# Optimization experiments

Measured on AMD Instinct MI355X. Metric: run time of the kernel, lower is better.

The kernel has to match this reference:

```python
import jax, jax.numpy as jnp
import numpy as np

D_MAX = 0.5      # max_dist init kwarg
EPS_W = 1e-8     # weight for far edges
EPS_L = 1e-5     # diagonal jitter on projected Laplacian


def setup_inputs() -> dict:
    key = jax.random.key(0)
    k1, k2, k3, k4, k5 = jax.random.split(key, 5)
    V, d_feat, E, K = 8192, 128, 262144, 512
    # scale so squared distances straddle D_MAX (both branches taken)
    inputs = jax.random.normal(k1, (V, d_feat), dtype=jnp.float32) * 0.05
    src = jax.random.randint(k2, (E,), 0, V)
    off = jax.random.randint(k3, (E,), 1, V)  # avoid self-loops
    dst = (src + off) % V
    edge_index = jnp.stack([src, dst]).astype(jnp.int32)
    A = jax.random.normal(k4, (K, K), dtype=jnp.float32)
    targets = A @ A.T / K + jnp.eye(K, dtype=jnp.float32)  # SPD covariance
    pmat = jax.random.normal(k5, (K, V), dtype=jnp.float32) / np.float32(np.sqrt(V))
    return {"inputs": inputs, "targets": targets, "edge_index": edge_index, "pmat": pmat}


def reference(inputs, targets, edge_index, pmat):
    V = inputs.shape[0]
    K = pmat.shape[0]
    src, dst = edge_index[0], edge_index[1]
    # vectorized per-edge squared distance + thresholded weight
    d = jnp.sum((inputs[src] - inputs[dst]) ** 2, axis=-1)            # [E]
    w = jnp.where(d <= D_MAX, jnp.exp(-d), jnp.float32(EPS_W))        # [E]
    # W = I on diag, w on (i,j) and (j,i) for edges, 0 elsewhere
    W = jnp.eye(V, dtype=inputs.dtype).at[src, dst].set(w).at[dst, src].set(w)
    deg = W.sum(axis=1)                                               # [V]
    idx = jnp.arange(V)
    L = (-W).at[idx, idx].add(deg)                                    # Laplacian D - W
    L_adj = (pmat @ L) @ pmat.T + EPS_L * jnp.eye(K, dtype=inputs.dtype)
    # log det(inv(L_adj)) = -logdet(L_adj); trace(L_adj @ S0) = sum(L_adj * S0^T)
    logdet_Ladj = jnp.linalg.slogdet(L_adj)[1]
    logdet_S0 = jnp.linalg.slogdet(targets)[1]
    tr = jnp.sum(L_adj * targets.T)
    return -logdet_Ladj - logdet_S0 - jnp.float32(K) + tr
```

## Files before the change

kernel.cpp:

```cpp
#include <hip/hip_runtime.h>
#include <math.h>

#define V_N 8192
#define D_F 128
#define E_N 262144
#define K_N 512
#define DMAXF 0.5f
#define EPSW 1e-8f
#define EPSL 1e-5f
#define MAX_SE 16384
#define NZ_SYRK 24
#define L68 68

#define NB_TR 1024
#define NB_CP 256
#define NB_ED (E_N / 32)

__global__ __launch_bounds__(256) void k_pre(const float* __restrict__ P, float* __restrict__ PT,
                                             const float* __restrict__ X, const int* __restrict__ ei,
                                             int* __restrict__ cnt, int* __restrict__ si,
                                             int* __restrict__ sj, float* __restrict__ sw,
                                             unsigned* __restrict__ htab,
                                             const float* __restrict__ T, float* __restrict__ Lw1) {
  int b = blockIdx.x, tid = threadIdx.x;
  if (b < NB_TR) {
    __shared__ float tl[64][65];
    int v0 = (b & 127) * 64, k0 = (b >> 7) * 64;
    int c4 = tid & 15, rq = tid >> 4;
#pragma unroll
    for (int rr = 0; rr < 4; ++rr) {
      int r = rq + 16 * rr;
      float4 f = *(const float4*)&P[(size_t)(k0 + r) * V_N + v0 + c4 * 4];
      tl[r][c4 * 4 + 0] = f.x; tl[r][c4 * 4 + 1] = f.y;
      tl[r][c4 * 4 + 2] = f.z; tl[r][c4 * 4 + 3] = f.w;
    }
    __syncthreads();
#pragma unroll
    for (int rr = 0; rr < 4; ++rr) {
      int r = rq + 16 * rr;
      float4 f;
      f.x = tl[c4 * 4 + 0][r]; f.y = tl[c4 * 4 + 1][r];
      f.z = tl[c4 * 4 + 2][r]; f.w = tl[c4 * 4 + 3][r];
      *(float4*)&PT[(size_t)(v0 + r) * K_N + k0 + c4 * 4] = f;
    }
  } else if (b < NB_TR + NB_CP) {
    int idx = (b - NB_TR) * 256 + tid;
    ((float4*)Lw1)[idx] = ((const float4*)T)[idx];
  } else {
    int t = (b - NB_TR - NB_CP) * 256 + tid;
    int e = t >> 3, lane = t & 7;
    int i = ei[e], j = ei[E_N + e];
    const float4* xi = (const float4*)(X + (size_t)i * D_F);
    const float4* xj = (const float4*)(X + (size_t)j * D_F);
    float4 A0 = xi[lane * 4 + 0], A1 = xi[lane * 4 + 1], A2 = xi[lane * 4 + 2], A3 = xi[lane * 4 + 3];
    float4 B0 = xj[lane * 4 + 0], B1 = xj[lane * 4 + 1], B2 = xj[lane * 4 + 2], B3 = xj[lane * 4 + 3];
    float d = 0.f, dx;
    dx = A0.x - B0.x; d += dx * dx; dx = A0.y - B0.y; d += dx * dx;
    dx = A0.z - B0.z; d += dx * dx; dx = A0.w - B0.w; d += dx * dx;
    dx = A1.x - B1.x; d += dx * dx; dx = A1.y - B1.y; d += dx * dx;
    dx = A1.z - B1.z; d += dx * dx; dx = A1.w - B1.w; d += dx * dx;
    dx = A2.x - B2.x; d += dx * dx; dx = A2.y - B2.y; d += dx * dx;
    dx = A2.z - B2.z; d += dx * dx; dx = A2.w - B2.w; d += dx * dx;
    dx = A3.x - B3.x; d += dx * dx; dx = A3.y - B3.y; d += dx * dx;
    dx = A3.z - B3.z; d += dx * dx; dx = A3.w - B3.w; d += dx * dx;
    d += __shfl_xor(d, 1);
    d += __shfl_xor(d, 2);
    d += __shfl_xor(d, 4);
    if (lane == 0 && d <= DMAXF) {
      float w = expf(-d);
      unsigned a = (unsigned)min(i, j), bb = (unsigned)max(i, j);
      unsigned key = a * 8192u + bb;
      unsigned h = (key * 2654435761u) >> 16;
      bool isnew = false;
      for (int probe = 0; probe < 65536; ++probe) {
        unsigned slot = (h + (unsigned)probe) & 65535u;
        unsigned prev = atomicCAS(&htab[slot], 0u, key);
        if (prev == 0u) { isnew = true; break; }
        if (prev == key) break;
      }
      if (isnew) {
        int p = atomicAdd(cnt, 1);
        if (p < MAX_SE) { si[p] = i; sj[p] = j; sw[p] = w; }
      }
    }
  }
}

__global__ __launch_bounds__(256) void k_syrk(const int* __restrict__ cnt, const int* __restrict__ si,
                                              const int* __restrict__ sj, const float* __restrict__ sw,
                                              const float* __restrict__ PT, float* __restrict__ La,
                                              const float* __restrict__ T, float* __restrict__ tr) {
  int p = blockIdx.x, bj = 0;
  while (p >= 8 - bj) { p -= 8 - bj; ++bj; }
  int bi = bj + p;
  int r0g = bi * 64, c0g = bj * 64;
  int m = min(*cnt, MAX_SE);
  int chunk = (m + NZ_SYRK - 1) / NZ_SYRK;
  int e0 = blockIdx.y * chunk;
  int e1 = min(m, e0 + chunk);

  __shared__ float As[16][68];
  __shared__ float Bs[16][68];
  int tid = threadIdx.x;
  int le = tid >> 4, f = tid & 15;
  int r0 = (tid >> 4) * 4, c0 = (tid & 15) * 4;
  float acc[4][4];
#pragma unroll
  for (int i = 0; i < 4; ++i)
#pragma unroll
    for (int j = 0; j < 4; ++j) acc[i][j] = 0.f;

  float w_ = 0.f;
  float4 ai = make_float4(0.f, 0.f, 0.f, 0.f), aj = ai, ci = ai, cj = ai;
  {
    int e = e0 + le;
    if (e < e1) {
      int i = si[e], j = sj[e];
      w_ = sw[e];
      const float* pi = &PT[(size_t)i * K_N];
      const float* pj = &PT[(size_t)j * K_N];
      ai = *(const float4*)(pi + r0g + f * 4);
      aj = *(const float4*)(pj + r0g + f * 4);
      if (bi != bj) {
        ci = *(const float4*)(pi + c0g + f * 4);
        cj = *(const float4*)(pj + c0g + f * 4);
      }
    }
  }

  for (int es = e0; es < e1; es += 16) {
    float sq = sqrtf(w_);
    float4 qa, qb;
    qa.x = sq * (ai.x - aj.x); qa.y = sq * (ai.y - aj.y);
    qa.z = sq * (ai.z - aj.z); qa.w = sq * (ai.w - aj.w);
    if (bi != bj) {
      qb.x = sq * (ci.x - cj.x); qb.y = sq * (ci.y - cj.y);
      qb.z = sq * (ci.z - cj.z); qb.w = sq * (ci.w - cj.w);
    } else {
      qb = qa;
    }
    __syncthreads();
    *(float4*)&As[le][f * 4] = qa;
    *(float4*)&Bs[le][f * 4] = qb;
    __syncthreads();

    {
      int e = es + 16 + le;
      w_ = 0.f;
      if (e < e1) {
        int i = si[e], j = sj[e];
        w_ = sw[e];
        const float* pi = &PT[(size_t)i * K_N];
        const float* pj = &PT[(size_t)j * K_N];
        ai = *(const float4*)(pi + r0g + f * 4);
        aj = *(const float4*)(pj + r0g + f * 4);
        if (bi != bj) {
          ci = *(const float4*)(pi + c0g + f * 4);
          cj = *(const float4*)(pj + c0g + f * 4);
        }
      }
    }

#pragma unroll
    for (int k = 0; k < 16; ++k) {
      float4 av = *(const float4*)&As[k][r0];
      float4 bv = *(const float4*)&Bs[k][c0];
      acc[0][0] += av.x * bv.x; acc[0][1] += av.x * bv.y; acc[0][2] += av.x * bv.z; acc[0][3] += av.x * bv.w;
      acc[1][0] += av.y * bv.x; acc[1][1] += av.y * bv.y; acc[1][2] += av.y * bv.z; acc[1][3] += av.y * bv.w;
      acc[2][0] += av.z * bv.x; acc[2][1] += av.z * bv.y; acc[2][2] += av.z * bv.z; acc[2][3] += av.z * bv.w;
      acc[3][0] += av.w * bv.x; acc[3][1] += av.w * bv.y; acc[3][2] += av.w * bv.z; acc[3][3] += av.w * bv.w;
    }
  }

  bool addeps = (blockIdx.y == 0) && (bi == bj);
  float tdot = 0.f;
#pragma unroll
  for (int i = 0; i < 4; ++i)
#pragma unroll
    for (int j = 0; j < 4; ++j) {
      float v = acc[i][j];
      int rg = r0g + r0 + i, cg = c0g + c0 + j;
      if (addeps && rg == cg) v += EPSL;
      atomicAdd(&La[(size_t)rg * K_N + cg], v);
      float sc = (bi != bj) ? 2.f : (rg == cg ? 1.f : (rg > cg ? 2.f : 0.f));
      if (sc != 0.f) tdot += sc * v * T[(size_t)rg * K_N + cg];
    }
  tdot += __shfl_down(tdot, 32); tdot += __shfl_down(tdot, 16); tdot += __shfl_down(tdot, 8);
  tdot += __shfl_down(tdot, 4);  tdot += __shfl_down(tdot, 2);  tdot += __shfl_down(tdot, 1);
  if ((tid & 63) == 0) atomicAdd(tr, tdot);
}

__device__ __forceinline__ void factor64_lds(const float* __restrict__ smF, float* A, int j0,
                                             float* __restrict__ ldout, int lane) {
  float a[64];
#pragma unroll
  for (int qq = 0; qq < 16; ++qq) {
    float4 f = *(const float4*)&smF[lane * L68 + qq * 4];
    a[qq * 4 + 0] = f.x; a[qq * 4 + 1] = f.y; a[qq * 4 + 2] = f.z; a[qq * 4 + 3] = f.w;
  }
  float ls = 0.f;
#pragma unroll
  for (int c = 0; c < 64; ++c) {
    float dc = __shfl(a[c], c);
    ls += logf(dc);
    float rs = rsqrtf(dc);
    a[c] *= rs;
#pragma unroll
    for (int k = c + 1; k < 64; ++k)
      a[k] -= a[c] * __shfl(a[c], k);
  }
#pragma unroll
  for (int qq = 0; qq < 16; ++qq) {
    float4 f;
    f.x = a[qq * 4 + 0]; f.y = a[qq * 4 + 1]; f.z = a[qq * 4 + 2]; f.w = a[qq * 4 + 3];
    *(float4*)&A[(size_t)(j0 + lane) * K_N + j0 + qq * 4] = f;
  }
  if (lane == 0) *ldout = ls;
}

__global__ __launch_bounds__(64) void k_fact0(float* La, float* Lw1, float* __restrict__ ld) {
  int m = blockIdx.x;
  float* A = m ? Lw1 : La;
  int lane = threadIdx.x;
  float a[64];
#pragma unroll
  for (int qq = 0; qq < 16; ++qq) {
    float4 f = *(const float4*)&A[(size_t)lane * K_N + qq * 4];
    a[qq * 4 + 0] = f.x; a[qq * 4 + 1] = f.y; a[qq * 4 + 2] = f.z; a[qq * 4 + 3] = f.w;
  }
  float ls = 0.f;
#pragma unroll
  for (int c = 0; c < 64; ++c) {
    float dc = __shfl(a[c], c);
    ls += logf(dc);
    float rs = rsqrtf(dc);
    a[c] *= rs;
#pragma unroll
    for (int k = c + 1; k < 64; ++k)
      a[k] -= a[c] * __shfl(a[c], k);
  }
#pragma unroll
  for (int qq = 0; qq < 16; ++qq) {
    float4 f;
    f.x = a[qq * 4 + 0]; f.y = a[qq * 4 + 1]; f.z = a[qq * 4 + 2]; f.w = a[qq * 4 + 3];
    *(float4*)&A[(size_t)lane * K_N + qq * 4] = f;
  }
  if (lane == 0) ld[m * 8] = ls;
}

__global__ __launch_bounds__(256, 1) void k_cstep(float* La, float* Lw1, float* __restrict__ ld, int s) {
  int m = blockIdx.y;
  float* A = m ? Lw1 : La;
  int tid = threadIdx.x;
  int nt2 = 7 - s;
  int q = blockIdx.x, lbj = 0;
  while (q >= nt2 - lbj) { q -= nt2 - lbj; ++lbj; }
  int lbi = lbj + q;
  int i = s + 1 + lbi, j = s + 1 + lbj;

  __shared__ float LT[64 * L68];
  __shared__ float PiT[64 * L68];
  __shared__ float PjT[64 * L68];
  __shared__ float rinv[64];

  for (int idx = tid; idx < 1024; idx += 256) {
    int r = idx >> 4, cq = (idx & 15) << 2;
    float4 f = *(const float4*)&A[(size_t)(s * 64 + r) * K_N + s * 64 + cq];
    LT[(cq + 0) * L68 + r] = f.x; LT[(cq + 1) * L68 + r] = f.y;
    LT[(cq + 2) * L68 + r] = f.z; LT[(cq + 3) * L68 + r] = f.w;
  }
  __syncthreads();
  if (tid < 64) rinv[tid] = 1.0f / LT[tid * L68 + tid];
  __syncthreads();

  {
    int w = tid >> 6, r = tid & 63;
    bool act = (w == 0) || (w == 1 && i != j);
    if (act) {
      int rowblk = (w == 0) ? i : j;
      const float* src = &A[(size_t)(rowblk * 64 + r) * K_N + s * 64];
      float x[64];
#pragma unroll
      for (int qq = 0; qq < 16; ++qq) {
        float4 f = *(const float4*)(src + qq * 4);
        x[qq * 4 + 0] = f.x; x[qq * 4 + 1] = f.y; x[qq * 4 + 2] = f.z; x[qq * 4 + 3] = f.w;
      }
#pragma unroll
      for (int c = 0; c < 64; ++c) {
        float xc = x[c] * rinv[c];
        x[c] = xc;
#pragma unroll
        for (int k = c + 1; k < 64; ++k)
          x[k] -= xc * LT[c * L68 + k];
      }
      float* dst = (w == 0) ? PiT : PjT;
#pragma unroll
      for (int k = 0; k < 64; ++k) dst[k * L68 + r] = x[k];
    }
  }
  __syncthreads();

  const float* Bp = (i == j) ? PiT : PjT;
  int r0 = (tid >> 4) * 4, c0 = (tid & 15) * 4;
  float acc[4][4];
#pragma unroll
  for (int ii = 0; ii < 4; ++ii)
#pragma unroll
    for (int jj = 0; jj < 4; ++jj) acc[ii][jj] = 0.f;
#pragma unroll 8
  for (int k = 0; k < 64; ++k) {
    float4 av = *(const float4*)&PiT[k * L68 + r0];
    float4 bv = *(const float4*)&Bp[k * L68 + c0];
    acc[0][0] += av.x * bv.x; acc[0][1] += av.x * bv.y; acc[0][2] += av.x * bv.z; acc[0][3] += av.x * bv.w;
    acc[1][0] += av.y * bv.x; acc[1][1] += av.y * bv.y; acc[1][2] += av.y * bv.z; acc[1][3] += av.y * bv.w;
    acc[2][0] += av.z * bv.x; acc[2][1] += av.z * bv.y; acc[2][2] += av.z * bv.z; acc[2][3] += av.z * bv.w;
    acc[3][0] += av.w * bv.x; acc[3][1] += av.w * bv.y; acc[3][2] += av.w * bv.z; acc[3][3] += av.w * bv.w;
  }

  if (i != j || i > s + 1) {
#pragma unroll
    for (int ii = 0; ii < 4; ++ii) {
      float* cp = &A[(size_t)(i * 64 + r0 + ii) * K_N + j * 64 + c0];
      float4 o = *(const float4*)cp;
      float4 wv;
      wv.x = o.x - acc[ii][0]; wv.y = o.y - acc[ii][1];
      wv.z = o.z - acc[ii][2]; wv.w = o.w - acc[ii][3];
      *(float4*)cp = wv;
    }
  } else {
#pragma unroll
    for (int ii = 0; ii < 4; ++ii) {
      const float* cp = &A[(size_t)(i * 64 + r0 + ii) * K_N + i * 64 + c0];
      float4 o = *(const float4*)cp;
      LT[(r0 + ii) * L68 + c0 + 0] = o.x - acc[ii][0];
      LT[(r0 + ii) * L68 + c0 + 1] = o.y - acc[ii][1];
      LT[(r0 + ii) * L68 + c0 + 2] = o.z - acc[ii][2];
      LT[(r0 + ii) * L68 + c0 + 3] = o.w - acc[ii][3];
    }
    __syncthreads();
    if (tid < 64)
      factor64_lds(LT, A, i * 64, &ld[m * 8 + s + 1], tid);
  }
}

__global__ void k_combine(const float* __restrict__ ld, const float* __restrict__ tr, float* __restrict__ out) {
  float l0 = 0.f, l1 = 0.f;
#pragma unroll
  for (int s = 0; s < 8; ++s) { l0 += ld[s]; l1 += ld[8 + s]; }
  out[0] = -l0 - l1 - (float)K_N + tr[0];
}

extern "C" void kernel_launch(void* const* d_in, const int* in_sizes, int n_in,
                              void* d_out, int out_size, void* d_ws, size_t ws_size,
                              hipStream_t stream) {
  const float* X  = (const float*)d_in[0];
  const float* T  = (const float*)d_in[1];
  const int*   ei = (const int*)d_in[2];
  const float* P  = (const float*)d_in[3];
  float* out = (float*)d_out;
  char* ws = (char*)d_ws;

  int*      cnt    = (int*)(ws + 0);
  float*    tr     = (float*)(ws + 16);
  float*    ld     = (float*)(ws + 32);
  unsigned* htab   = (unsigned*)(ws + 4096);
  float*    La     = (float*)(ws + 266240);
  float*    Lw1    = (float*)(ws + 1314816);
  int*      si     = (int*)(ws + 2363392);
  int*      sj     = (int*)(ws + 2428928);
  float*    sw     = (float*)(ws + 2494464);
  float*    PT     = (float*)(ws + 2560000);

  hipMemsetAsync(ws, 0, 1314816, stream);

  k_pre<<<NB_TR + NB_CP + NB_ED, 256, 0, stream>>>(P, PT, X, ei, cnt, si, sj, sw, htab, T, Lw1);
  k_syrk<<<dim3(36, NZ_SYRK), 256, 0, stream>>>(cnt, si, sj, sw, PT, La, T, tr);

  k_fact0<<<2, 64, 0, stream>>>(La, Lw1, ld);
  for (int s = 0; s < 7; ++s) {
    int nt2 = 7 - s;
    k_cstep<<<dim3(nt2 * (nt2 + 1) / 2, 2), 256, 0, stream>>>(La, Lw1, ld, s);
  }
  k_combine<<<1, 1, 0, stream>>>(ld, tr, out);
}
```

Before: 549.8 us.

## Enlarge SYRK tiles to 128x128 and split Cholesky step into TRSM and update kernels

The SYRK kernel now computes 128x128 output tiles with an 8x8 per-thread micro-tile, which cuts redundant gathers of projected rows. It doubles the edge-split factor to keep the grid occupied and hoists the sqrt of the weights out of the loop. The blocked Cholesky step is split into a per-block-row TRSM kernel followed by an update kernel, so each panel is solved once instead of being recomputed in every update tile. This adds an extra launch per step and raises register pressure in SYRK.

```diff
diff --git a/kernel.cpp b/kernel.cpp
--- a/kernel.cpp
+++ b/kernel.cpp
@@ -9,7 +9,7 @@
 #define EPSW 1e-8f
 #define EPSL 1e-5f
 #define MAX_SE 16384
-#define NZ_SYRK 24
+#define NZ_SYRK 48
 #define L68 68
 
 #define NB_TR 1024
@@ -91,57 +91,69 @@
                                               const float* __restrict__ PT, float* __restrict__ La,
                                               const float* __restrict__ T, float* __restrict__ tr) {
   int p = blockIdx.x, bj = 0;
-  while (p >= 8 - bj) { p -= 8 - bj; ++bj; }
+  while (p >= 4 - bj) { p -= 4 - bj; ++bj; }
   int bi = bj + p;
-  int r0g = bi * 64, c0g = bj * 64;
+  int r0g = bi * 128, c0g = bj * 128;
+  bool diag = (bi == bj);
   int m = min(*cnt, MAX_SE);
   int chunk = (m + NZ_SYRK - 1) / NZ_SYRK;
   int e0 = blockIdx.y * chunk;
   int e1 = min(m, e0 + chunk);
 
-  __shared__ float As[16][68];
-  __shared__ float Bs[16][68];
+  __shared__ float As[16][132];
+  __shared__ float Bs[16][132];
   int tid = threadIdx.x;
-  int le = tid >> 4, f = tid & 15;
-  int r0 = (tid >> 4) * 4, c0 = (tid & 15) * 4;
-  float acc[4][4];
-#pragma unroll
-  for (int i = 0; i < 4; ++i)
-#pragma unroll
-    for (int j = 0; j < 4; ++j) acc[i][j] = 0.f;
+  int le = tid >> 4, f2 = tid & 15;
+  int r0 = (tid >> 4) * 8, c0 = (tid & 15) * 8;
+  float acc[8][8];
+#pragma unroll
+  for (int ii = 0; ii < 8; ++ii)
+#pragma unroll
+    for (int jj = 0; jj < 8; ++jj) acc[ii][jj] = 0.f;
 
   float w_ = 0.f;
-  float4 ai = make_float4(0.f, 0.f, 0.f, 0.f), aj = ai, ci = ai, cj = ai;
+  float4 z4 = make_float4(0.f, 0.f, 0.f, 0.f);
+  float4 ra0 = z4, ra1 = z4, rb0 = z4, rb1 = z4;
+  float4 ca0 = z4, ca1 = z4, cb0 = z4, cb1 = z4;
   {
     int e = e0 + le;
     if (e < e1) {
       int i = si[e], j = sj[e];
-      w_ = sw[e];
+      w_ = sqrtf(sw[e]);
       const float* pi = &PT[(size_t)i * K_N];
       const float* pj = &PT[(size_t)j * K_N];
-      ai = *(const float4*)(pi + r0g + f * 4);
-      aj = *(const float4*)(pj + r0g + f * 4);
-      if (bi != bj) {
-        ci = *(const float4*)(pi + c0g + f * 4);
-        cj = *(const float4*)(pj + c0g + f * 4);
+      ra0 = *(const float4*)(pi + r0g + f2 * 8);
+      ra1 = *(const float4*)(pi + r0g + f2 * 8 + 4);
+      rb0 = *(const float4*)(pj + r0g + f2 * 8);
+      rb1 = *(const float4*)(pj + r0g + f2 * 8 + 4);
+      if (!diag) {
+        ca0 = *(const float4*)(pi + c0g + f2 * 8);
+        ca1 = *(const float4*)(pi + c0g + f2 * 8 + 4);
+        cb0 = *(const float4*)(pj + c0g + f2 * 8);
+        cb1 = *(const float4*)(pj + c0g + f2 * 8 + 4);
       }
     }
   }
 
   for (int es = e0; es < e1; es += 16) {
-    float sq = sqrtf(w_);
-    float4 qa, qb;
-    qa.x = sq * (ai.x - aj.x); qa.y = sq * (ai.y - aj.y);
-    qa.z = sq * (ai.z - aj.z); qa.w = sq * (ai.w - aj.w);
-    if (bi != bj) {
-      qb.x = sq * (ci.x - cj.x); qb.y = sq * (ci.y - cj.y);
-      qb.z = sq * (ci.z - cj.z); qb.w = sq * (ci.w - cj.w);
-    } else {
-      qb = qa;
+    float4 qa0, qa1, qb0, qb1;
+    qa0.x = w_ * (ra0.x - rb0.x); qa0.y = w_ * (ra0.y - rb0.y);
+    qa0.z = w_ * (ra0.z - rb0.z); qa0.w = w_ * (ra0.w - rb0.w);
+    qa1.x = w_ * (ra1.x - rb1.x); qa1.y = w_ * (ra1.y - rb1.y);
+    qa1.z = w_ * (ra1.z - rb1.z); qa1.w = w_ * (ra1.w - rb1.w);
+    if (!diag) {
+      qb0.x = w_ * (ca0.x - cb0.x); qb0.y = w_ * (ca0.y - cb0.y);
+      qb0.z = w_ * (ca0.z - cb0.z); qb0.w = w_ * (ca0.w - cb0.w);
+      qb1.x = w_ * (ca1.x - cb1.x); qb1.y = w_ * (ca1.y - cb1.y);
+      qb1.z = w_ * (ca1.z - cb1.z); qb1.w = w_ * (ca1.w - cb1.w);
     }
     __syncthreads();
-    *(float4*)&As[le][f * 4] = qa;
-    *(float4*)&Bs[le][f * 4] = qb;
+    *(float4*)&As[le][f2 * 8] = qa0;
+    *(float4*)&As[le][f2 * 8 + 4] = qa1;
+    if (!diag) {
+      *(float4*)&Bs[le][f2 * 8] = qb0;
+      *(float4*)&Bs[le][f2 * 8 + 4] = qb1;
+    }
     __syncthreads();
 
     {
@@ -149,40 +161,53 @@
       w_ = 0.f;
       if (e < e1) {
         int i = si[e], j = sj[e];
-        w_ = sw[e];
+        w_ = sqrtf(sw[e]);
         const float* pi = &PT[(size_t)i * K_N];
         const float* pj = &PT[(size_t)j * K_N];
-        ai = *(const float4*)(pi + r0g + f * 4);
-        aj = *(const float4*)(pj + r0g + f * 4);
-        if (bi != bj) {
-          ci = *(const float4*)(pi + c0g + f * 4);
-          cj = *(const float4*)(pj + c0g + f * 4);
+        ra0 = *(const float4*)(pi + r0g + f2 * 8);
+        ra1 = *(const float4*)(pi + r0g + f2 * 8 + 4);
+        rb0 = *(const float4*)(pj + r0g + f2 * 8);
+        rb1 = *(const float4*)(pj + r0g + f2 * 8 + 4);
+        if (!diag) {
+          ca0 = *(const float4*)(pi + c0g + f2 * 8);
+          ca1 = *(const float4*)(pi + c0g + f2 * 8 + 4);
+          cb0 = *(const float4*)(pj + c0g + f2 * 8);
+          cb1 = *(const float4*)(pj + c0g + f2 * 8 + 4);
         }
       }
     }
 
+    const float(*Bp)[132] = diag ? As : Bs;
 #pragma unroll
     for (int k = 0; k < 16; ++k) {
-      float4 av = *(const float4*)&As[k][r0];
-      float4 bv = *(const float4*)&Bs[k][c0];
-      acc[0][0] += av.x * bv.x; acc[0][1] += av.x * bv.y; acc[0][2] += av.x * bv.z; acc[0][3] += av.x * bv.w;
-      acc[1][0] += av.y * bv.x; acc[1][1] += av.y * bv.y; acc[1][2] += av.y * bv.z; acc[1][3] += av.y * bv.w;
-      acc[2][0] += av.z * bv.x; acc[2][1] += av.z * bv.y; acc[2][2] += av.z * bv.z; acc[2][3] += av.z * bv.w;
-      acc[3][0] += av.w * bv.x; acc[3][1] += av.w * bv.y; acc[3][2] += av.w * bv.z; acc[3][3] += av.w * bv.w;
-    }
-  }
-
-  bool addeps = (blockIdx.y == 0) && (bi == bj);
+      float av[8], bv[8];
+      float4 a0 = *(const float4*)&As[k][r0];
+      float4 a1 = *(const float4*)&As[k][r0 + 4];
+      float4 b0 = *(const float4*)&Bp[k][c0];
+      float4 b1 = *(const float4*)&Bp[k][c0 + 4];
+      av[0] = a0.x; av[1] = a0.y; av[2] = a0.z; av[3] = a0.w;
+      av[4] = a1.x; av[5] = a1.y; av[6] = a1.z; av[7] = a1.w;
+      bv[0] = b0.x; bv[1] = b0.y; bv[2] = b0.z; bv[3] = b0.w;
+      bv[4] = b1.x; bv[5] = b1.y; bv[6] = b1.z; bv[7] = b1.w;
+#pragma unroll
+      for (int ii = 0; ii < 8; ++ii)
+#pragma unroll
+        for (int jj = 0; jj < 8; ++jj)
+          acc[ii][jj] += av[ii] * bv[jj];
+    }
+  }
+
+  bool addeps = (blockIdx.y == 0) && diag;
   float tdot = 0.f;
 #pragma unroll
-  for (int i = 0; i < 4; ++i)
-#pragma unroll
-    for (int j = 0; j < 4; ++j) {
-      float v = acc[i][j];
-      int rg = r0g + r0 + i, cg = c0g + c0 + j;
+  for (int ii = 0; ii < 8; ++ii)
+#pragma unroll
+    for (int jj = 0; jj < 8; ++jj) {
+      float v = acc[ii][jj];
+      int rg = r0g + r0 + ii, cg = c0g + c0 + jj;
       if (addeps && rg == cg) v += EPSL;
       atomicAdd(&La[(size_t)rg * K_N + cg], v);
-      float sc = (bi != bj) ? 2.f : (rg == cg ? 1.f : (rg > cg ? 2.f : 0.f));
+      float sc = !diag ? 2.f : (rg == cg ? 1.f : (rg > cg ? 2.f : 0.f));
       if (sc != 0.f) tdot += sc * v * T[(size_t)rg * K_N + cg];
     }
   tdot += __shfl_down(tdot, 32); tdot += __shfl_down(tdot, 16); tdot += __shfl_down(tdot, 8);
@@ -248,7 +273,55 @@
   if (lane == 0) ld[m * 8] = ls;
 }
 
-__global__ __launch_bounds__(256, 1) void k_cstep(float* La, float* Lw1, float* __restrict__ ld, int s) {
+__global__ __launch_bounds__(64) void k_trsm(float* La, float* Lw1, int s) {
+  int m = blockIdx.y;
+  float* A = m ? Lw1 : La;
+  int i = s + 1 + blockIdx.x;
+  int lane = threadIdx.x;
+  __shared__ float LT[64 * L68];
+  __shared__ float rinv[64];
+
+  for (int idx = lane; idx < 1024; idx += 64) {
+    int r = idx >> 4, cq = (idx & 15) << 2;
+    float4 f = *(const float4*)&A[(size_t)(s * 64 + r) * K_N + s * 64 + cq];
+    LT[(cq + 0) * L68 + r] = f.x; LT[(cq + 1) * L68 + r] = f.y;
+    LT[(cq + 2) * L68 + r] = f.z; LT[(cq + 3) * L68 + r] = f.w;
+  }
+  __syncthreads();
+  rinv[lane] = 1.0f / LT[lane * L68 + lane];
+  __syncthreads();
+
+  float x[64];
+  const float* src = &A[(size_t)(i * 64 + lane) * K_N + s * 64];
+#pragma unroll
+  for (int qq = 0; qq < 16; ++qq) {
+    float4 f = *(const float4*)(src + qq * 4);
+    x[qq * 4 + 0] = f.x; x[qq * 4 + 1] = f.y; x[qq * 4 + 2] = f.z; x[qq * 4 + 3] = f.w;
+  }
+#pragma unroll
+  for (int c = 0; c < 64; ++c) {
+    float xc = x[c] * rinv[c];
+    x[c] = xc;
+    int kk = c + 1;
+#pragma unroll
+    for (; kk < 64 && (kk & 3); ++kk) x[kk] -= xc * LT[c * L68 + kk];
+#pragma unroll
+    for (; kk < 64; kk += 4) {
+      float4 f = *(const float4*)&LT[c * L68 + kk];
+      x[kk + 0] -= xc * f.x; x[kk + 1] -= xc * f.y;
+      x[kk + 2] -= xc * f.z; x[kk + 3] -= xc * f.w;
+    }
+  }
+  float* dst = &A[(size_t)(i * 64 + lane) * K_N + s * 64];
+#pragma unroll
+  for (int qq = 0; qq < 16; ++qq) {
+    float4 f;
+    f.x = x[qq * 4 + 0]; f.y = x[qq * 4 + 1]; f.z = x[qq * 4 + 2]; f.w = x[qq * 4 + 3];
+    *(float4*)(dst + qq * 4) = f;
+  }
+}
+
+__global__ __launch_bounds__(256) void k_upd(float* La, float* Lw1, float* __restrict__ ld, int s) {
   int m = blockIdx.y;
   float* A = m ? Lw1 : La;
   int tid = threadIdx.x;
@@ -258,44 +331,18 @@
   int lbi = lbj + q;
   int i = s + 1 + lbi, j = s + 1 + lbj;
 
-  __shared__ float LT[64 * L68];
   __shared__ float PiT[64 * L68];
   __shared__ float PjT[64 * L68];
-  __shared__ float rinv[64];
 
   for (int idx = tid; idx < 1024; idx += 256) {
-    int r = idx >> 4, cq = (idx & 15) << 2;
-    float4 f = *(const float4*)&A[(size_t)(s * 64 + r) * K_N + s * 64 + cq];
-    LT[(cq + 0) * L68 + r] = f.x; LT[(cq + 1) * L68 + r] = f.y;
-    LT[(cq + 2) * L68 + r] = f.z; LT[(cq + 3) * L68 + r] = f.w;
-  }
-  __syncthreads();
-  if (tid < 64) rinv[tid] = 1.0f / LT[tid * L68 + tid];
-  __syncthreads();
-
-  {
-    int w = tid >> 6, r = tid & 63;
-    bool act = (w == 0) || (w == 1 && i != j);
-    if (act) {
-      int rowblk = (w == 0) ? i : j;
-      const float* src = &A[(size_t)(rowblk * 64 + r) * K_N + s * 64];
-      float x[64];
-#pragma unroll
-      for (int qq = 0; qq < 16; ++qq) {
-        float4 f = *(const float4*)(src + qq * 4);
-        x[qq * 4 + 0] = f.x; x[qq * 4 + 1] = f.y; x[qq * 4 + 2] = f.z; x[qq * 4 + 3] = f.w;
-      }
-#pragma unroll
-      for (int c = 0; c < 64; ++c) {
-        float xc = x[c] * rinv[c];
-        x[c] = xc;
-#pragma unroll
-        for (int k = c + 1; k < 64; ++k)
-          x[k] -= xc * LT[c * L68 + k];
-      }
-      float* dst = (w == 0) ? PiT : PjT;
-#pragma unroll
-      for (int k = 0; k < 64; ++k) dst[k * L68 + r] = x[k];
+    int r = idx >> 4, kq = (idx & 15) << 2;
+    float4 f = *(const float4*)&A[(size_t)(i * 64 + r) * K_N + s * 64 + kq];
+    PiT[(kq + 0) * L68 + r] = f.x; PiT[(kq + 1) * L68 + r] = f.y;
+    PiT[(kq + 2) * L68 + r] = f.z; PiT[(kq + 3) * L68 + r] = f.w;
+    if (i != j) {
+      float4 g = *(const float4*)&A[(size_t)(j * 64 + r) * K_N + s * 64 + kq];
+      PjT[(kq + 0) * L68 + r] = g.x; PjT[(kq + 1) * L68 + r] = g.y;
+      PjT[(kq + 2) * L68 + r] = g.z; PjT[(kq + 3) * L68 + r] = g.w;
     }
   }
   __syncthreads();
@@ -332,14 +379,14 @@
     for (int ii = 0; ii < 4; ++ii) {
       const float* cp = &A[(size_t)(i * 64 + r0 + ii) * K_N + i * 64 + c0];
       float4 o = *(const float4*)cp;
-      LT[(r0 + ii) * L68 + c0 + 0] = o.x - acc[ii][0];
-      LT[(r0 + ii) * L68 + c0 + 1] = o.y - acc[ii][1];
-      LT[(r0 + ii) * L68 + c0 + 2] = o.z - acc[ii][2];
-      LT[(r0 + ii) * L68 + c0 + 3] = o.w - acc[ii][3];
+      PjT[(r0 + ii) * L68 + c0 + 0] = o.x - acc[ii][0];
+      PjT[(r0 + ii) * L68 + c0 + 1] = o.y - acc[ii][1];
+      PjT[(r0 + ii) * L68 + c0 + 2] = o.z - acc[ii][2];
+      PjT[(r0 + ii) * L68 + c0 + 3] = o.w - acc[ii][3];
     }
     __syncthreads();
     if (tid < 64)
-      factor64_lds(LT, A, i * 64, &ld[m * 8 + s + 1], tid);
+      factor64_lds(PjT, A, i * 64, &ld[m * 8 + s + 1], tid);
   }
 }
 
@@ -374,12 +421,13 @@
   hipMemsetAsync(ws, 0, 1314816, stream);
 
   k_pre<<<NB_TR + NB_CP + NB_ED, 256, 0, stream>>>(P, PT, X, ei, cnt, si, sj, sw, htab, T, Lw1);
-  k_syrk<<<dim3(36, NZ_SYRK), 256, 0, stream>>>(cnt, si, sj, sw, PT, La, T, tr);
+  k_syrk<<<dim3(10, NZ_SYRK), 256, 0, stream>>>(cnt, si, sj, sw, PT, La, T, tr);
 
   k_fact0<<<2, 64, 0, stream>>>(La, Lw1, ld);
   for (int s = 0; s < 7; ++s) {
     int nt2 = 7 - s;
-    k_cstep<<<dim3(nt2 * (nt2 + 1) / 2, 2), 256, 0, stream>>>(La, Lw1, ld, s);
+    k_trsm<<<dim3(nt2, 2), 64, 0, stream>>>(La, Lw1, s);
+    k_upd<<<dim3(nt2 * (nt2 + 1) / 2, 2), 256, 0, stream>>>(La, Lw1, ld, s);
   }
   k_combine<<<1, 1, 0, stream>>>(ld, tr, out);
 }
```

Measured after the change: 1.146 ms. +108.5%, slower.

## Fuse first diagonal factor and final combine into Cholesky step kernels

Applied to the files above, without the earlier changes.

Removes the separate k_fact0 and k_combine launches. Each s=0 step block now factors the first 64x64 diagonal tile redundantly in registers, and the last step uses an atomic completion counter so one block writes the final scalar. The edge-distance stage now uses 4 lanes per edge instead of 8, and the triangular-solve inner loop reads LDS as float4. This saves two kernel launches at the cost of redundant diagonal factorizations and an atomic-based final reduction.

```diff
diff --git a/kernel.cpp b/kernel.cpp
--- a/kernel.cpp
+++ b/kernel.cpp
@@ -14,7 +14,7 @@
 
 #define NB_TR 1024
 #define NB_CP 256
-#define NB_ED (E_N / 32)
+#define NB_ED (E_N / 64)
 
 __global__ __launch_bounds__(256) void k_pre(const float* __restrict__ P, float* __restrict__ PT,
                                              const float* __restrict__ X, const int* __restrict__ ei,
@@ -48,24 +48,23 @@
     ((float4*)Lw1)[idx] = ((const float4*)T)[idx];
   } else {
     int t = (b - NB_TR - NB_CP) * 256 + tid;
-    int e = t >> 3, lane = t & 7;
+    int e = t >> 2, lane = t & 3;
     int i = ei[e], j = ei[E_N + e];
     const float4* xi = (const float4*)(X + (size_t)i * D_F);
     const float4* xj = (const float4*)(X + (size_t)j * D_F);
-    float4 A0 = xi[lane * 4 + 0], A1 = xi[lane * 4 + 1], A2 = xi[lane * 4 + 2], A3 = xi[lane * 4 + 3];
-    float4 B0 = xj[lane * 4 + 0], B1 = xj[lane * 4 + 1], B2 = xj[lane * 4 + 2], B3 = xj[lane * 4 + 3];
-    float d = 0.f, dx;
-    dx = A0.x - B0.x; d += dx * dx; dx = A0.y - B0.y; d += dx * dx;
-    dx = A0.z - B0.z; d += dx * dx; dx = A0.w - B0.w; d += dx * dx;
-    dx = A1.x - B1.x; d += dx * dx; dx = A1.y - B1.y; d += dx * dx;
-    dx = A1.z - B1.z; d += dx * dx; dx = A1.w - B1.w; d += dx * dx;
-    dx = A2.x - B2.x; d += dx * dx; dx = A2.y - B2.y; d += dx * dx;
-    dx = A2.z - B2.z; d += dx * dx; dx = A2.w - B2.w; d += dx * dx;
-    dx = A3.x - B3.x; d += dx * dx; dx = A3.y - B3.y; d += dx * dx;
-    dx = A3.z - B3.z; d += dx * dx; dx = A3.w - B3.w; d += dx * dx;
+    float d = 0.f;
+#pragma unroll
+    for (int q = 0; q < 8; ++q) {
+      float4 a = xi[lane * 8 + q];
+      float4 bb = xj[lane * 8 + q];
+      float dx;
+      dx = a.x - bb.x; d += dx * dx;
+      dx = a.y - bb.y; d += dx * dx;
+      dx = a.z - bb.z; d += dx * dx;
+      dx = a.w - bb.w; d += dx * dx;
+    }
     d += __shfl_xor(d, 1);
     d += __shfl_xor(d, 2);
-    d += __shfl_xor(d, 4);
     if (lane == 0 && d <= DMAXF) {
       float w = expf(-d);
       unsigned a = (unsigned)min(i, j), bb = (unsigned)max(i, j);
@@ -218,37 +217,9 @@
   if (lane == 0) *ldout = ls;
 }
 
-__global__ __launch_bounds__(64) void k_fact0(float* La, float* Lw1, float* __restrict__ ld) {
-  int m = blockIdx.x;
-  float* A = m ? Lw1 : La;
-  int lane = threadIdx.x;
-  float a[64];
-#pragma unroll
-  for (int qq = 0; qq < 16; ++qq) {
-    float4 f = *(const float4*)&A[(size_t)lane * K_N + qq * 4];
-    a[qq * 4 + 0] = f.x; a[qq * 4 + 1] = f.y; a[qq * 4 + 2] = f.z; a[qq * 4 + 3] = f.w;
-  }
-  float ls = 0.f;
-#pragma unroll
-  for (int c = 0; c < 64; ++c) {
-    float dc = __shfl(a[c], c);
-    ls += logf(dc);
-    float rs = rsqrtf(dc);
-    a[c] *= rs;
-#pragma unroll
-    for (int k = c + 1; k < 64; ++k)
-      a[k] -= a[c] * __shfl(a[c], k);
-  }
-#pragma unroll
-  for (int qq = 0; qq < 16; ++qq) {
-    float4 f;
-    f.x = a[qq * 4 + 0]; f.y = a[qq * 4 + 1]; f.z = a[qq * 4 + 2]; f.w = a[qq * 4 + 3];
-    *(float4*)&A[(size_t)lane * K_N + qq * 4] = f;
-  }
-  if (lane == 0) ld[m * 8] = ls;
-}
-
-__global__ __launch_bounds__(256, 1) void k_cstep(float* La, float* Lw1, float* __restrict__ ld, int s) {
+__global__ __launch_bounds__(256, 1) void k_cstep(float* La, float* Lw1, float* __restrict__ ld,
+                                                  const float* __restrict__ tr, float* __restrict__ out,
+                                                  unsigned* __restrict__ donec, int s) {
   int m = blockIdx.y;
   float* A = m ? Lw1 : La;
   int tid = threadIdx.x;
@@ -263,13 +234,39 @@
   __shared__ float PjT[64 * L68];
   __shared__ float rinv[64];
 
-  for (int idx = tid; idx < 1024; idx += 256) {
-    int r = idx >> 4, cq = (idx & 15) << 2;
-    float4 f = *(const float4*)&A[(size_t)(s * 64 + r) * K_N + s * 64 + cq];
-    LT[(cq + 0) * L68 + r] = f.x; LT[(cq + 1) * L68 + r] = f.y;
-    LT[(cq + 2) * L68 + r] = f.z; LT[(cq + 3) * L68 + r] = f.w;
-  }
-  __syncthreads();
+  if (s == 0) {
+    if (tid < 64) {
+      float a[64];
+#pragma unroll
+      for (int qq = 0; qq < 16; ++qq) {
+        float4 f = *(const float4*)&A[(size_t)tid * K_N + qq * 4];
+        a[qq * 4 + 0] = f.x; a[qq * 4 + 1] = f.y; a[qq * 4 + 2] = f.z; a[qq * 4 + 3] = f.w;
+      }
+      float ls = 0.f;
+#pragma unroll
+      for (int c = 0; c < 64; ++c) {
+        float dc = __shfl(a[c], c);
+        ls += logf(dc);
+        float rs = rsqrtf(dc);
+        a[c] *= rs;
+#pragma unroll
+        for (int k = c + 1; k < 64; ++k)
+          a[k] -= a[c] * __shfl(a[c], k);
+      }
+#pragma unroll
+      for (int c = 0; c < 64; ++c) LT[c * L68 + tid] = a[c];
+      if (i == 1 && j == 1 && tid == 0) ld[m * 8] = ls;
+    }
+    __syncthreads();
+  } else {
+    for (int idx = tid; idx < 1024; idx += 256) {
+      int r = idx >> 4, cq = (idx & 15) << 2;
+      float4 f = *(const float4*)&A[(size_t)(s * 64 + r) * K_N + s * 64 + cq];
+      LT[(cq + 0) * L68 + r] = f.x; LT[(cq + 1) * L68 + r] = f.y;
+      LT[(cq + 2) * L68 + r] = f.z; LT[(cq + 3) * L68 + r] = f.w;
+    }
+    __syncthreads();
+  }
   if (tid < 64) rinv[tid] = 1.0f / LT[tid * L68 + tid];
   __syncthreads();
 
@@ -289,9 +286,15 @@
       for (int c = 0; c < 64; ++c) {
         float xc = x[c] * rinv[c];
         x[c] = xc;
-#pragma unroll
-        for (int k = c + 1; k < 64; ++k)
-          x[k] -= xc * LT[c * L68 + k];
+        int kk = c + 1;
+#pragma unroll
+        for (; kk < 64 && (kk & 3); ++kk) x[kk] -= xc * LT[c * L68 + kk];
+#pragma unroll
+        for (; kk < 64; kk += 4) {
+          float4 f = *(const float4*)&LT[c * L68 + kk];
+          x[kk + 0] -= xc * f.x; x[kk + 1] -= xc * f.y;
+          x[kk + 2] -= xc * f.z; x[kk + 3] -= xc * f.w;
+        }
       }
       float* dst = (w == 0) ? PiT : PjT;
 #pragma unroll
@@ -332,22 +335,28 @@
     for (int ii = 0; ii < 4; ++ii) {
       const float* cp = &A[(size_t)(i * 64 + r0 + ii) * K_N + i * 64 + c0];
       float4 o = *(const float4*)cp;
-      LT[(r0 + ii) * L68 + c0 + 0] = o.x - acc[ii][0];
-      LT[(r0 + ii) * L68 + c0 + 1] = o.y - acc[ii][1];
-      LT[(r0 + ii) * L68 + c0 + 2] = o.z - acc[ii][2];
-      LT[(r0 + ii) * L68 + c0 + 3] = o.w - acc[ii][3];
+      PjT[(r0 + ii) * L68 + c0 + 0] = o.x - acc[ii][0];
+      PjT[(r0 + ii) * L68 + c0 + 1] = o.y - acc[ii][1];
+      PjT[(r0 + ii) * L68 + c0 + 2] = o.z - acc[ii][2];
+      PjT[(r0 + ii) * L68 + c0 + 3] = o.w - acc[ii][3];
     }
     __syncthreads();
     if (tid < 64)
-      factor64_lds(LT, A, i * 64, &ld[m * 8 + s + 1], tid);
-  }
-}
-
-__global__ void k_combine(const float* __restrict__ ld, const float* __restrict__ tr, float* __restrict__ out) {
-  float l0 = 0.f, l1 = 0.f;
-#pragma unroll
-  for (int s = 0; s < 8; ++s) { l0 += ld[s]; l1 += ld[8 + s]; }
-  out[0] = -l0 - l1 - (float)K_N + tr[0];
+      factor64_lds(PjT, A, i * 64, &ld[m * 8 + s + 1], tid);
+
+    if (s == 6 && tid == 0) {
+      __threadfence();
+      unsigned old = __hip_atomic_fetch_add(donec, 1u, __ATOMIC_ACQ_REL, __HIP_MEMORY_SCOPE_AGENT);
+      if (old == 1u) {
+        float lsum = 0.f;
+#pragma unroll
+        for (int t = 0; t < 16; ++t)
+          lsum += __hip_atomic_load(&ld[t], __ATOMIC_ACQUIRE, __HIP_MEMORY_SCOPE_AGENT);
+        float trv = __hip_atomic_load(tr, __ATOMIC_ACQUIRE, __HIP_MEMORY_SCOPE_AGENT);
+        out[0] = -lsum - (float)K_N + trv;
+      }
+    }
+  }
 }
 
 extern "C" void kernel_launch(void* const* d_in, const int* in_sizes, int n_in,
@@ -363,6 +372,7 @@
   int*      cnt    = (int*)(ws + 0);
   float*    tr     = (float*)(ws + 16);
   float*    ld     = (float*)(ws + 32);
+  unsigned* donec  = (unsigned*)(ws + 192);
   unsigned* htab   = (unsigned*)(ws + 4096);
   float*    La     = (float*)(ws + 266240);
   float*    Lw1    = (float*)(ws + 1314816);
@@ -376,10 +386,8 @@
   k_pre<<<NB_TR + NB_CP + NB_ED, 256, 0, stream>>>(P, PT, X, ei, cnt, si, sj, sw, htab, T, Lw1);
   k_syrk<<<dim3(36, NZ_SYRK), 256, 0, stream>>>(cnt, si, sj, sw, PT, La, T, tr);
 
-  k_fact0<<<2, 64, 0, stream>>>(La, Lw1, ld);
   for (int s = 0; s < 7; ++s) {
     int nt2 = 7 - s;
-    k_cstep<<<dim3(nt2 * (nt2 + 1) / 2, 2), 256, 0, stream>>>(La, Lw1, ld, s);
-  }
-  k_combine<<<1, 1, 0, stream>>>(ld, tr, out);
-}
+    k_cstep<<<dim3(nt2 * (nt2 + 1) / 2, 2), 256, 0, stream>>>(La, Lw1, ld, tr, out, donec, s);
+  }
+}
```

New measurement: 789.7 us. +43.6%, slower.

## Fuse last Cholesky steps and final combine into one LDS-resident tail kernel

Applied to the files above, without the earlier changes.

Replaces the last two blocked-Cholesky step launches and the combine kernel with a single k_tail kernel per matrix. It keeps the remaining 3 tiles in LDS and finishes the factorization there, then sums the log-determinants through an atomic counter in the last-finishing block. It also vectorizes the triangular-solve LDS reads with float4 and adds an asm barrier to force early issue of the edge-feature loads. This removes two launches and their global round trips, at the cost of roughly 100KB of LDS and a mostly serial tail run by one wave.

```diff
diff --git a/kernel.cpp b/kernel.cpp
--- a/kernel.cpp
+++ b/kernel.cpp
@@ -54,6 +54,8 @@
     const float4* xj = (const float4*)(X + (size_t)j * D_F);
     float4 A0 = xi[lane * 4 + 0], A1 = xi[lane * 4 + 1], A2 = xi[lane * 4 + 2], A3 = xi[lane * 4 + 3];
     float4 B0 = xj[lane * 4 + 0], B1 = xj[lane * 4 + 1], B2 = xj[lane * 4 + 2], B3 = xj[lane * 4 + 3];
+    asm volatile("" :: "v"(A0.x), "v"(A1.x), "v"(A2.x), "v"(A3.x),
+                       "v"(B0.x), "v"(B1.x), "v"(B2.x), "v"(B3.x));
     float d = 0.f, dx;
     dx = A0.x - B0.x; d += dx * dx; dx = A0.y - B0.y; d += dx * dx;
     dx = A0.z - B0.z; d += dx * dx; dx = A0.w - B0.w; d += dx * dx;
@@ -190,14 +192,7 @@
   if ((tid & 63) == 0) atomicAdd(tr, tdot);
 }
 
-__device__ __forceinline__ void factor64_lds(const float* __restrict__ smF, float* A, int j0,
-                                             float* __restrict__ ldout, int lane) {
-  float a[64];
-#pragma unroll
-  for (int qq = 0; qq < 16; ++qq) {
-    float4 f = *(const float4*)&smF[lane * L68 + qq * 4];
-    a[qq * 4 + 0] = f.x; a[qq * 4 + 1] = f.y; a[qq * 4 + 2] = f.z; a[qq * 4 + 3] = f.w;
-  }
+__device__ __forceinline__ float factor64_shfl(float a[64]) {
   float ls = 0.f;
 #pragma unroll
   for (int c = 0; c < 64; ++c) {
@@ -209,6 +204,18 @@
     for (int k = c + 1; k < 64; ++k)
       a[k] -= a[c] * __shfl(a[c], k);
   }
+  return ls;
+}
+
+__device__ __forceinline__ void factor64_lds(const float* __restrict__ smF, float* A, int j0,
+                                             float* __restrict__ ldout, int lane) {
+  float a[64];
+#pragma unroll
+  for (int qq = 0; qq < 16; ++qq) {
+    float4 f = *(const float4*)&smF[lane * L68 + qq * 4];
+    a[qq * 4 + 0] = f.x; a[qq * 4 + 1] = f.y; a[qq * 4 + 2] = f.z; a[qq * 4 + 3] = f.w;
+  }
+  float ls = factor64_shfl(a);
 #pragma unroll
   for (int qq = 0; qq < 16; ++qq) {
     float4 f;
@@ -228,17 +235,7 @@
     float4 f = *(const float4*)&A[(size_t)lane * K_N + qq * 4];
     a[qq * 4 + 0] = f.x; a[qq * 4 + 1] = f.y; a[qq * 4 + 2] = f.z; a[qq * 4 + 3] = f.w;
   }
-  float ls = 0.f;
-#pragma unroll
-  for (int c = 0; c < 64; ++c) {
-    float dc = __shfl(a[c], c);
-    ls += logf(dc);
-    float rs = rsqrtf(dc);
-    a[c] *= rs;
-#pragma unroll
-    for (int k = c + 1; k < 64; ++k)
-      a[k] -= a[c] * __shfl(a[c], k);
-  }
+  float ls = factor64_shfl(a);
 #pragma unroll
   for (int qq = 0; qq < 16; ++qq) {
     float4 f;
@@ -289,9 +286,15 @@
       for (int c = 0; c < 64; ++c) {
         float xc = x[c] * rinv[c];
         x[c] = xc;
-#pragma unroll
-        for (int k = c + 1; k < 64; ++k)
-          x[k] -= xc * LT[c * L68 + k];
+        int kk = c + 1;
+#pragma unroll
+        for (; kk < 64 && (kk & 3); ++kk) x[kk] -= xc * LT[c * L68 + kk];
+#pragma unroll
+        for (; kk < 64; kk += 4) {
+          float4 f = *(const float4*)&LT[c * L68 + kk];
+          x[kk + 0] -= xc * f.x; x[kk + 1] -= xc * f.y;
+          x[kk + 2] -= xc * f.z; x[kk + 3] -= xc * f.w;
+        }
       }
       float* dst = (w == 0) ? PiT : PjT;
 #pragma unroll
@@ -332,22 +335,168 @@
     for (int ii = 0; ii < 4; ++ii) {
       const float* cp = &A[(size_t)(i * 64 + r0 + ii) * K_N + i * 64 + c0];
       float4 o = *(const float4*)cp;
-      LT[(r0 + ii) * L68 + c0 + 0] = o.x - acc[ii][0];
-      LT[(r0 + ii) * L68 + c0 + 1] = o.y - acc[ii][1];
-      LT[(r0 + ii) * L68 + c0 + 2] = o.z - acc[ii][2];
-      LT[(r0 + ii) * L68 + c0 + 3] = o.w - acc[ii][3];
+      PjT[(r0 + ii) * L68 + c0 + 0] = o.x - acc[ii][0];
+      PjT[(r0 + ii) * L68 + c0 + 1] = o.y - acc[ii][1];
+      PjT[(r0 + ii) * L68 + c0 + 2] = o.z - acc[ii][2];
+      PjT[(r0 + ii) * L68 + c0 + 3] = o.w - acc[ii][3];
     }
     __syncthreads();
     if (tid < 64)
-      factor64_lds(LT, A, i * 64, &ld[m * 8 + s + 1], tid);
-  }
-}
-
-__global__ void k_combine(const float* __restrict__ ld, const float* __restrict__ tr, float* __restrict__ out) {
-  float l0 = 0.f, l1 = 0.f;
-#pragma unroll
-  for (int s = 0; s < 8; ++s) { l0 += ld[s]; l1 += ld[8 + s]; }
-  out[0] = -l0 - l1 - (float)K_N + tr[0];
+      factor64_lds(PjT, A, i * 64, &ld[m * 8 + s + 1], tid);
+  }
+}
+
+__device__ __forceinline__ void upd_tile_lds(float* __restrict__ U, const float* __restrict__ Pi,
+                                             const float* __restrict__ Pj, int tid) {
+  int r0 = (tid >> 4) * 4, c0 = (tid & 15) * 4;
+  float acc[4][4];
+#pragma unroll
+  for (int ii = 0; ii < 4; ++ii)
+#pragma unroll
+    for (int jj = 0; jj < 4; ++jj) acc[ii][jj] = 0.f;
+#pragma unroll 8
+  for (int k = 0; k < 64; ++k) {
+    float4 av = *(const float4*)&Pi[k * L68 + r0];
+    float4 bv = *(const float4*)&Pj[k * L68 + c0];
+    acc[0][0] += av.x * bv.x; acc[0][1] += av.x * bv.y; acc[0][2] += av.x * bv.z; acc[0][3] += av.x * bv.w;
+    acc[1][0] += av.y * bv.x; acc[1][1] += av.y * bv.y; acc[1][2] += av.y * bv.z; acc[1][3] += av.y * bv.w;
+    acc[2][0] += av.z * bv.x; acc[2][1] += av.z * bv.y; acc[2][2] += av.z * bv.z; acc[2][3] += av.z * bv.w;
+    acc[3][0] += av.w * bv.x; acc[3][1] += av.w * bv.y; acc[3][2] += av.w * bv.z; acc[3][3] += av.w * bv.w;
+  }
+#pragma unroll
+  for (int ii = 0; ii < 4; ++ii)
+#pragma unroll
+    for (int jj = 0; jj < 4; ++jj)
+      U[(r0 + ii) * L68 + c0 + jj] -= acc[ii][jj];
+}
+
+__global__ __launch_bounds__(256, 1) void k_tail(float* La, float* Lw1, float* __restrict__ ld,
+                                                 const float* __restrict__ tr, float* __restrict__ out,
+                                                 unsigned* __restrict__ donec) {
+  int m = blockIdx.x;
+  float* A = m ? Lw1 : La;
+  int tid = threadIdx.x;
+  __shared__ float LT[64 * L68];
+  __shared__ float P6s[64 * L68];
+  __shared__ float P7s[64 * L68];
+  __shared__ float U66[64 * L68];
+  __shared__ float U76[64 * L68];
+  __shared__ float U77[64 * L68];
+  __shared__ float rinv[64];
+
+  for (int idx = tid; idx < 1024; idx += 256) {
+    int r = idx >> 4, cq = (idx & 15) << 2;
+    float4 f = *(const float4*)&A[(size_t)(320 + r) * K_N + 320 + cq];
+    LT[(cq + 0) * L68 + r] = f.x; LT[(cq + 1) * L68 + r] = f.y;
+    LT[(cq + 2) * L68 + r] = f.z; LT[(cq + 3) * L68 + r] = f.w;
+    *(float4*)&U66[r * L68 + cq] = *(const float4*)&A[(size_t)(384 + r) * K_N + 384 + cq];
+    *(float4*)&U76[r * L68 + cq] = *(const float4*)&A[(size_t)(448 + r) * K_N + 384 + cq];
+    *(float4*)&U77[r * L68 + cq] = *(const float4*)&A[(size_t)(448 + r) * K_N + 448 + cq];
+  }
+  __syncthreads();
+  if (tid < 64) rinv[tid] = 1.0f / LT[tid * L68 + tid];
+  __syncthreads();
+
+  {
+    int w = tid >> 6, r = tid & 63;
+    if (w < 2) {
+      const float* src = &A[(size_t)((w ? 448 : 384) + r) * K_N + 320];
+      float x[64];
+#pragma unroll
+      for (int qq = 0; qq < 16; ++qq) {
+        float4 f = *(const float4*)(src + qq * 4);
+        x[qq * 4 + 0] = f.x; x[qq * 4 + 1] = f.y; x[qq * 4 + 2] = f.z; x[qq * 4 + 3] = f.w;
+      }
+#pragma unroll
+      for (int c = 0; c < 64; ++c) {
+        float xc = x[c] * rinv[c];
+        x[c] = xc;
+        int kk = c + 1;
+#pragma unroll
+        for (; kk < 64 && (kk & 3); ++kk) x[kk] -= xc * LT[c * L68 + kk];
+#pragma unroll
+        for (; kk < 64; kk += 4) {
+          float4 f = *(const float4*)&LT[c * L68 + kk];
+          x[kk + 0] -= xc * f.x; x[kk + 1] -= xc * f.y;
+          x[kk + 2] -= xc * f.z; x[kk + 3] -= xc * f.w;
+        }
+      }
+      float* dst = w ? P7s : P6s;
+#pragma unroll
+      for (int k = 0; k < 64; ++k) dst[k * L68 + r] = x[k];
+    }
+  }
+  __syncthreads();
+
+  upd_tile_lds(U66, P6s, P6s, tid);
+  upd_tile_lds(U76, P7s, P6s, tid);
+  upd_tile_lds(U77, P7s, P7s, tid);
+  __syncthreads();
+
+  if (tid < 64) {
+    float a[64];
+#pragma unroll
+    for (int qq = 0; qq < 16; ++qq) {
+      float4 f = *(const float4*)&U66[tid * L68 + qq * 4];
+      a[qq * 4 + 0] = f.x; a[qq * 4 + 1] = f.y; a[qq * 4 + 2] = f.z; a[qq * 4 + 3] = f.w;
+    }
+    float ls = factor64_shfl(a);
+#pragma unroll
+    for (int c = 0; c < 64; ++c) LT[c * L68 + tid] = a[c];
+    if (tid == 0) ld[m * 8 + 6] = ls;
+    rinv[tid] = 1.0f / LT[tid * L68 + tid];
+  }
+  if (tid < 64) {
+    float x[64];
+#pragma unroll
+    for (int qq = 0; qq < 16; ++qq) {
+      float4 f = *(const float4*)&U76[tid * L68 + qq * 4];
+      x[qq * 4 + 0] = f.x; x[qq * 4 + 1] = f.y; x[qq * 4 + 2] = f.z; x[qq * 4 + 3] = f.w;
+    }
+#pragma unroll
+    for (int c = 0; c < 64; ++c) {
+      float xc = x[c] * rinv[c];
+      x[c] = xc;
+      int kk = c + 1;
+#pragma unroll
+      for (; kk < 64 && (kk & 3); ++kk) x[kk] -= xc * LT[c * L68 + kk];
+#pragma unroll
+      for (; kk < 64; kk += 4) {
+        float4 f = *(const float4*)&LT[c * L68 + kk];
+        x[kk + 0] -= xc * f.x; x[kk + 1] -= xc * f.y;
+        x[kk + 2] -= xc * f.z; x[kk + 3] -= xc * f.w;
+      }
+    }
+#pragma unroll
+    for (int k = 0; k < 64; ++k) P6s[k * L68 + tid] = x[k];
+  }
+  __syncthreads();
+
+  upd_tile_lds(U77, P6s, P6s, tid);
+  __syncthreads();
+
+  if (tid < 64) {
+    float a[64];
+#pragma unroll
+    for (int qq = 0; qq < 16; ++qq) {
+      float4 f = *(const float4*)&U77[tid * L68 + qq * 4];
+      a[qq * 4 + 0] = f.x; a[qq * 4 + 1] = f.y; a[qq * 4 + 2] = f.z; a[qq * 4 + 3] = f.w;
+    }
+    float ls = factor64_shfl(a);
+    if (tid == 0) {
+      ld[m * 8 + 7] = ls;
+      __threadfence();
+      unsigned old = __hip_atomic_fetch_add(donec, 1u, __ATOMIC_ACQ_REL, __HIP_MEMORY_SCOPE_AGENT);
+      if (old == 1u) {
+        float lsum = 0.f;
+#pragma unroll
+        for (int t = 0; t < 16; ++t)
+          lsum += __hip_atomic_load(&ld[t], __ATOMIC_ACQUIRE, __HIP_MEMORY_SCOPE_AGENT);
+        float trv = __hip_atomic_load(tr, __ATOMIC_ACQUIRE, __HIP_MEMORY_SCOPE_AGENT);
+        out[0] = -lsum - (float)K_N + trv;
+      }
+    }
+  }
 }
 
 extern "C" void kernel_launch(void* const* d_in, const int* in_sizes, int n_in,
@@ -363,6 +512,7 @@
   int*      cnt    = (int*)(ws + 0);
   float*    tr     = (float*)(ws + 16);
   float*    ld     = (float*)(ws + 32);
+  unsigned* donec  = (unsigned*)(ws + 192);
   unsigned* htab   = (unsigned*)(ws + 4096);
   float*    La     = (float*)(ws + 266240);
   float*    Lw1    = (float*)(ws + 1314816);
@@ -377,9 +527,9 @@
   k_syrk<<<dim3(36, NZ_SYRK), 256, 0, stream>>>(cnt, si, sj, sw, PT, La, T, tr);
 
   k_fact0<<<2, 64, 0, stream>>>(La, Lw1, ld);
-  for (int s = 0; s < 7; ++s) {
+  for (int s = 0; s < 5; ++s) {
     int nt2 = 7 - s;
     k_cstep<<<dim3(nt2 * (nt2 + 1) / 2, 2), 256, 0, stream>>>(La, Lw1, ld, s);
   }
-  k_combine<<<1, 1, 0, stream>>>(ld, tr, out);
-}
+  k_tail<<<2, 256, 0, stream>>>(La, Lw1, ld, tr, out, donec);
+}
```

Measured after the change: 784.9 us. 1.43x slower.
